# Kernel tuning notes

Measured on AMD Instinct MI355X. Metric: run time of the kernel, lower is better.

Reference implementation:

```python
import jax, jax.numpy as jnp
import numpy as np

N, F_IN, F_OUT = 20000, 512, 512
E = 320000
S = 6           # max_subgraph_size
T = 0.5         # evolution_time
HSCALE = 0.05   # Hamiltonian scale
MAX_TERMS = 4   # truncated matrix-exp series terms
EPS = 1e-5      # BatchNorm eps


def _build_subgraphs(edge_index_np):
    # deterministic stand-in for SubgraphCache: 1-hop in-neighbors, center first,
    # truncated to S nodes (matches mapping=0 after subsampling in the original)
    loops = np.stack([np.arange(N), np.arange(N)])
    ei = np.concatenate([edge_index_np.astype(np.int64), loops], axis=1)
    codes = np.unique(ei[0] * N + ei[1])   # dedup directed edges incl. self loops
    src, dst = codes // N, codes % N
    order = np.argsort(dst, kind='stable')
    src_s, dst_s = src[order], dst[order]
    starts = np.searchsorted(dst_s, np.arange(N))
    ends = np.searchsorted(dst_s, np.arange(N) + 1)
    sub_nodes = np.zeros((N, S), dtype=np.int32)
    valid = np.zeros((N, S), dtype=bool)
    for i in range(N):
        nb = np.unique(src_s[starts[i]:ends[i]])
        nb = nb[nb != i][:S - 1]
        k = 1 + nb.shape[0]
        sub_nodes[i, 0] = i
        sub_nodes[i, 1:k] = nb
        valid[i, :k] = True
    # induced directed adjacency of each size-S subgraph (padded slots zeroed)
    pair = sub_nodes[:, :, None].astype(np.int64) * N + sub_nodes[:, None, :].astype(np.int64)
    hit = np.isin(pair, codes)
    pv = valid[:, :, None] & valid[:, None, :]
    sub_adj = (hit & pv).astype(np.int32)
    return jnp.asarray(sub_nodes), jnp.asarray(sub_adj)


def setup_inputs() -> dict:
    key = jax.random.key(0)
    ks = jax.random.split(key, 4)
    x = jax.random.normal(ks[0], (N, F_IN), dtype=jnp.float32)
    edge_index = jax.random.randint(ks[1], (2, E), 0, N, dtype=jnp.int32)
    sub_nodes, sub_adj = _build_subgraphs(np.asarray(edge_index))
    W_re = jax.random.normal(ks[2], (F_IN, F_OUT), dtype=jnp.float32) * 0.02
    W_im = jax.random.normal(ks[3], (F_IN, F_OUT), dtype=jnp.float32) * 0.02
    b_re = jnp.zeros((F_OUT,), jnp.float32)
    b_im = jnp.zeros((F_OUT,), jnp.float32)
    gamma_r = jnp.ones((F_OUT,), jnp.float32)
    beta_r = jnp.zeros((F_OUT,), jnp.float32)
    gamma_i = jnp.ones((F_OUT,), jnp.float32)
    beta_i = jnp.zeros((F_OUT,), jnp.float32)
    return {"x": x, "edge_index": edge_index, "sub_nodes": sub_nodes,
            "sub_adj": sub_adj, "W_re": W_re, "W_im": W_im, "b_re": b_re,
            "b_im": b_im, "gamma_r": gamma_r, "beta_r": beta_r,
            "gamma_i": gamma_i, "beta_i": beta_i}


def _bn(v, gamma, beta):
    # training-mode BatchNorm1d (biased variance), applied per real/imag part
    mu = v.mean(axis=0)
    var = jnp.var(v, axis=0)
    return (v - mu) * jax.lax.rsqrt(var + EPS) * gamma + beta


def reference(x, edge_index, sub_nodes, sub_adj, W_re, W_im, b_re, b_im,
              gamma_r, beta_r, gamma_i, beta_i):
    # ComplexLinear on real-valued input: y = x @ (W_re + i W_im) + b
    y = jax.lax.complex(x @ W_re + b_re, x @ W_im + b_im)    # [N, F_OUT] c64
    # per-node subgraph Laplacian Hamiltonian: L = diag(deg) - A, H = 0.05 * L
    A = sub_adj.astype(jnp.float32)                          # [N, S, S]
    deg = A.sum(-1)                                          # degree(row)
    L = deg[:, :, None] * jnp.eye(S, dtype=jnp.float32) - A
    scaled = (-1j * T * HSCALE) * L.astype(jnp.complex64)    # -i * H * t
    # center row (index 0) of truncated series exp(-iHt); lower block of the
    # 2dim unitary hits zero-padded z rows, so only U_sub row 0 matters
    v = jnp.zeros((N, S), jnp.complex64).at[:, 0].set(1.0)
    term, res = v, v
    for k in range(1, MAX_TERMS + 1):
        term = jnp.einsum('ns,nst->nt', term, scaled) / k
        res = res + term
    sub_x = y[sub_nodes]                                     # [N, S, F_OUT]
    evolved = jnp.einsum('ns,nsf->nf', res, sub_x)           # center of U @ z
    # complex ReLU -> naive complex BatchNorm -> residual (in==out, no proj)
    er, ei = jax.nn.relu(evolved.real), jax.nn.relu(evolved.imag)
    out_r = _bn(er, gamma_r, beta_r) + x
    out_i = _bn(ei, gamma_i, beta_i)
    # complex output represented as concat(real, imag)
    return jnp.concatenate([out_r, out_i], axis=-1)          # [N, 2*F_OUT]
```

## Files before the change

kernel.cpp:

```cpp
#include <hip/hip_runtime.h>

#define N_NODES 20000
#define FDIM 512
#define SSZ 6

typedef __attribute__((ext_vector_type(8))) short bf16x8;
typedef __attribute__((ext_vector_type(4))) float f32x4;
typedef __attribute__((ext_vector_type(8))) unsigned short u16x8;

static __device__ __forceinline__ unsigned short f2bf(float f) {
    unsigned int u = __float_as_uint(f);
    unsigned int r = (u + 0x7fffu + ((u >> 16) & 1u)) >> 16;
    return (unsigned short)r;
}
static __device__ __forceinline__ float bf2f(unsigned short u) {
    return __uint_as_float(((unsigned int)u) << 16);
}

__global__ __launch_bounds__(256) void conv_all(
    const float* __restrict__ x, const float* __restrict__ Wre,
    const float* __restrict__ Wim, unsigned short* __restrict__ xb,
    unsigned short* __restrict__ wt, float* __restrict__ sums)
{
    const int blk = blockIdx.x;
    const int tid = threadIdx.x;
    if (blk < 5000) {
        const size_t i = ((size_t)blk * 256 + tid) * 8;
        const float4 a = *(const float4*)(x + i);
        const float4 b = *(const float4*)(x + i + 4);
        u16x8 o;
        o[0] = f2bf(a.x); o[1] = f2bf(a.y); o[2] = f2bf(a.z); o[3] = f2bf(a.w);
        o[4] = f2bf(b.x); o[5] = f2bf(b.y); o[6] = f2bf(b.z); o[7] = f2bf(b.w);
        *(u16x8*)(xb + i) = o;
    } else if (blk < 5512) {
        __shared__ float tile[32][33];
        const int bidx = blk - 5000;
        const int z = bidx >> 8;
        const int rem = bidx & 255;
        const int k0 = (rem & 15) * 32;
        const int n0 = (rem >> 4) * 32;
        const float* W = z ? Wim : Wre;
        const int tx = tid & 31, ty = tid >> 5;
#pragma unroll
        for (int i = 0; i < 4; ++i)
            tile[ty + i * 8][tx] = W[(size_t)(k0 + ty + i * 8) * FDIM + n0 + tx];
        __syncthreads();
        unsigned short* wtb = wt + (size_t)z * FDIM * FDIM;
#pragma unroll
        for (int i = 0; i < 4; ++i)
            wtb[(size_t)(n0 + ty + i * 8) * FDIM + k0 + tx] = f2bf(tile[tx][ty + i * 8]);
    } else {
#pragma unroll
        for (int i = 0; i < 8; ++i) sums[i * 256 + tid] = 0.f;
    }
}

#define BM 64
#define BN 128
#define BK 64

__global__ __launch_bounds__(256) void gemm_mfma(
    const unsigned short* __restrict__ xb,
    const unsigned short* __restrict__ wt,
    const float* __restrict__ bre, const float* __restrict__ bim,
    unsigned short* __restrict__ y)
{
    __shared__ __align__(16) unsigned short lA[BM * BK];
    __shared__ __align__(16) unsigned short lB[BN * BK];

    const int tid  = threadIdx.x;
    const int wave = tid >> 6;
    const int lane = tid & 63;
    const int rowBase = blockIdx.y * BM;
    const int colBase = blockIdx.x * BN;

    const int wm = (wave >> 1) * 32;
    const int wn = (wave & 1) * 64;

    f32x4 acc[2][4];
#pragma unroll
    for (int i = 0; i < 2; ++i)
#pragma unroll
        for (int j = 0; j < 4; ++j) acc[i][j] = (f32x4){0.f, 0.f, 0.f, 0.f};

    const int srow   = lane >> 3;
    const int schunk = lane & 7;
    const int gchunk = schunk ^ srow;

    const int fm = lane & 15;
    const int kq = lane >> 4;

    for (int k0 = 0; k0 < FDIM; k0 += BK) {
#pragma unroll
        for (int i = 0; i < 2; ++i) {
            const int trow = wave * 16 + i * 8;
            int grow = rowBase + trow + srow;
            if (grow > N_NODES - 1) grow = N_NODES - 1;
            const unsigned short* gp = xb + (size_t)grow * FDIM + k0 + gchunk * 8;
            __builtin_amdgcn_global_load_lds(
                (const __attribute__((address_space(1))) void*)gp,
                (__attribute__((address_space(3))) void*)(lA + trow * BK), 16, 0, 0);
        }
#pragma unroll
        for (int i = 0; i < 4; ++i) {
            const int trow = wave * 32 + i * 8;
            const int grow = colBase + trow + srow;
            const unsigned short* gp = wt + (size_t)grow * FDIM + k0 + gchunk * 8;
            __builtin_amdgcn_global_load_lds(
                (const __attribute__((address_space(1))) void*)gp,
                (__attribute__((address_space(3))) void*)(lB + trow * BK), 16, 0, 0);
        }
        __syncthreads();

#pragma unroll
        for (int ks = 0; ks < 2; ++ks) {
            bf16x8 af[2], bfr[4];
            const int g = ks * 4 + kq;
#pragma unroll
            for (int mt = 0; mt < 2; ++mt) {
                const int row = wm + mt * 16 + fm;
                af[mt] = *(const bf16x8*)&lA[row * BK + ((g ^ (row & 7)) << 3)];
            }
#pragma unroll
            for (int nt = 0; nt < 4; ++nt) {
                const int row = wn + nt * 16 + fm;
                bfr[nt] = *(const bf16x8*)&lB[row * BK + ((g ^ (row & 7)) << 3)];
            }
#pragma unroll
            for (int mt = 0; mt < 2; ++mt)
#pragma unroll
                for (int nt = 0; nt < 4; ++nt)
                    acc[mt][nt] = __builtin_amdgcn_mfma_f32_16x16x32_bf16(
                        af[mt], bfr[nt], acc[mt][nt], 0, 0, 0);
        }
        __syncthreads();
    }

    const int rquad = lane >> 4;
#pragma unroll
    for (int nt = 0; nt < 4; ++nt) {
        const int col = colBase + wn + nt * 16 + fm;
        const float bias = (col < FDIM) ? bre[col] : bim[col - FDIM];
#pragma unroll
        for (int mt = 0; mt < 2; ++mt) {
            const int row0 = rowBase + wm + mt * 16 + rquad * 4;
#pragma unroll
            for (int r = 0; r < 4; ++r) {
                const int row = row0 + r;
                if (row < N_NODES)
                    y[(size_t)row * 1024 + col] = f2bf(acc[mt][nt][r] + bias);
            }
        }
    }
}

__global__ __launch_bounds__(256) void evolve_stats(
    const unsigned short* __restrict__ y,
    const int* __restrict__ sub_nodes,
    const int* __restrict__ sub_adj,
    unsigned short* __restrict__ eb,
    float* __restrict__ sums)
{
    __shared__ float lsum[2048];
    const int wave = threadIdx.x >> 6;
    const int lane = threadIdx.x & 63;
    const int f = lane << 3;

    float sR[8] = {0.f}, sR2[8] = {0.f}, sI[8] = {0.f}, sI2[8] = {0.f};

    for (int q = 0; q < 4; ++q) {
        const int n = blockIdx.x * 16 + wave * 4 + q;

        const int* sa = sub_adj + (size_t)n * (SSZ * SSZ);
        float A[SSZ][SSZ], deg[SSZ];
#pragma unroll
        for (int s = 0; s < SSZ; ++s) {
            float d = 0.f;
#pragma unroll
            for (int t = 0; t < SSZ; ++t) { float a = (float)sa[s * SSZ + t]; A[s][t] = a; d += a; }
            deg[s] = d;
        }
        float p1[SSZ], p2[SSZ], p3[SSZ], p4[SSZ];
#pragma unroll
        for (int t = 0; t < SSZ; ++t) p1[t] = ((t == 0) ? deg[0] : 0.f) - A[0][t];
#pragma unroll
        for (int t = 0; t < SSZ; ++t) {
            float acc = 0.f;
#pragma unroll
            for (int s = 0; s < SSZ; ++s) acc += p1[s] * (((s == t) ? deg[s] : 0.f) - A[s][t]);
            p2[t] = acc;
        }
#pragma unroll
        for (int t = 0; t < SSZ; ++t) {
            float acc = 0.f;
#pragma unroll
            for (int s = 0; s < SSZ; ++s) acc += p2[s] * (((s == t) ? deg[s] : 0.f) - A[s][t]);
            p3[t] = acc;
        }
#pragma unroll
        for (int t = 0; t < SSZ; ++t) {
            float acc = 0.f;
#pragma unroll
            for (int s = 0; s < SSZ; ++s) acc += p3[s] * (((s == t) ? deg[s] : 0.f) - A[s][t]);
            p4[t] = acc;
        }
        float rre[SSZ], rim[SSZ];
#pragma unroll
        for (int t = 0; t < SSZ; ++t) {
            rre[t] = ((t == 0) ? 1.f : 0.f) - 3.125e-4f * p2[t] + 1.6276041666666668e-8f * p4[t];
            rim[t] = -0.025f * p1[t] + 2.6041666666666666e-6f * p3[t];
        }

        float aR[8] = {0.f}, aI[8] = {0.f};
#pragma unroll
        for (int s = 0; s < SSZ; ++s) {
            const int nd = sub_nodes[n * SSZ + s];
            const float cr = rre[s], ci = rim[s];
            const unsigned short* base = y + (size_t)nd * 1024 + f;
            const u16x8 yr8 = *(const u16x8*)base;
            const u16x8 yi8 = *(const u16x8*)(base + FDIM);
#pragma unroll
            for (int j = 0; j < 8; ++j) {
                const float yr = bf2f(yr8[j]);
                const float yi = bf2f(yi8[j]);
                aR[j] = fmaf(cr, yr, fmaf(-ci, yi, aR[j]));
                aI[j] = fmaf(cr, yi, fmaf(ci, yr, aI[j]));
            }
        }
        u16x8 er8, ei8;
#pragma unroll
        for (int j = 0; j < 8; ++j) {
            const unsigned short re = f2bf(fmaxf(aR[j], 0.f));
            const unsigned short im = f2bf(fmaxf(aI[j], 0.f));
            er8[j] = re; ei8[j] = im;
            const float erv = bf2f(re), eiv = bf2f(im);
            sR[j] += erv;  sR2[j] = fmaf(erv, erv, sR2[j]);
            sI[j] += eiv;  sI2[j] = fmaf(eiv, eiv, sI2[j]);
        }
        *(u16x8*)(eb + (size_t)n * 1024 + f) = er8;
        *(u16x8*)(eb + (size_t)n * 1024 + FDIM + f) = ei8;
    }

    if (wave == 0) {
#pragma unroll
        for (int j = 0; j < 8; ++j) {
            lsum[f + j] = sR[j];  lsum[512 + f + j] = sR2[j];
            lsum[1024 + f + j] = sI[j];  lsum[1536 + f + j] = sI2[j];
        }
    }
    for (int w = 1; w < 4; ++w) {
        __syncthreads();
        if (wave == w) {
#pragma unroll
            for (int j = 0; j < 8; ++j) {
                lsum[f + j] += sR[j];  lsum[512 + f + j] += sR2[j];
                lsum[1024 + f + j] += sI[j];  lsum[1536 + f + j] += sI2[j];
            }
        }
    }
    __syncthreads();
#pragma unroll
    for (int i = 0; i < 8; ++i) {
        const int idx = i * 256 + threadIdx.x;
        atomicAdd(&sums[idx], lsum[idx]);
    }
}

__global__ __launch_bounds__(256) void finalize_kernel(
    const float* __restrict__ x, const unsigned short* __restrict__ eb,
    const float* __restrict__ sums,
    const float* __restrict__ gr, const float* __restrict__ br_,
    const float* __restrict__ gi, const float* __restrict__ bi_,
    float* __restrict__ out)
{
    const int gid = blockIdx.x * 256 + threadIdx.x;
    const int n = gid >> 6;
    const int f = (gid & 63) << 3;
    const float invN = 1.0f / (float)N_NODES;

    float scr[8], shr[8], sci[8], shi[8];
#pragma unroll
    for (int h = 0; h < 2; ++h) {
        const int fo = f + h * 4;
        const float4 s1 = *(const float4*)(sums + fo);
        const float4 s2 = *(const float4*)(sums + 512 + fo);
        const float4 s3 = *(const float4*)(sums + 1024 + fo);
        const float4 s4 = *(const float4*)(sums + 1536 + fo);
        const float4 g1 = *(const float4*)(gr + fo);
        const float4 b1 = *(const float4*)(br_ + fo);
        const float4 g2 = *(const float4*)(gi + fo);
        const float4 b2 = *(const float4*)(bi_ + fo);
        const float mu[4] = {s1.x * invN, s1.y * invN, s1.z * invN, s1.w * invN};
        const float q2[4] = {s2.x * invN, s2.y * invN, s2.z * invN, s2.w * invN};
        const float mi[4] = {s3.x * invN, s3.y * invN, s3.z * invN, s3.w * invN};
        const float qi[4] = {s4.x * invN, s4.y * invN, s4.z * invN, s4.w * invN};
        const float gg1[4] = {g1.x, g1.y, g1.z, g1.w};
        const float bb1[4] = {b1.x, b1.y, b1.z, b1.w};
        const float gg2[4] = {g2.x, g2.y, g2.z, g2.w};
        const float bb2[4] = {b2.x, b2.y, b2.z, b2.w};
#pragma unroll
        for (int j = 0; j < 4; ++j) {
            const float vr = fmaf(-mu[j], mu[j], q2[j]);
            const float sc1 = rsqrtf(vr + 1e-5f) * gg1[j];
            scr[h * 4 + j] = sc1;
            shr[h * 4 + j] = fmaf(-mu[j], sc1, bb1[j]);
            const float vi = fmaf(-mi[j], mi[j], qi[j]);
            const float sc2 = rsqrtf(vi + 1e-5f) * gg2[j];
            sci[h * 4 + j] = sc2;
            shi[h * 4 + j] = fmaf(-mi[j], sc2, bb2[j]);
        }
    }

    const u16x8 er8 = *(const u16x8*)(eb + (size_t)n * 1024 + f);
    const u16x8 ei8 = *(const u16x8*)(eb + (size_t)n * 1024 + FDIM + f);
    float orr[8], oii[8];
#pragma unroll
    for (int j = 0; j < 8; ++j) {
        const float xv = x[(size_t)n * FDIM + f + j];
        orr[j] = fmaf(bf2f(er8[j]), scr[j], shr[j]) + xv;
        oii[j] = fmaf(bf2f(ei8[j]), sci[j], shi[j]);
    }
#pragma unroll
    for (int j = 0; j < 8; j += 4) {
        *(float4*)(out + (size_t)n * 1024 + f + j) =
            make_float4(orr[j], orr[j + 1], orr[j + 2], orr[j + 3]);
        *(float4*)(out + (size_t)n * 1024 + FDIM + f + j) =
            make_float4(oii[j], oii[j + 1], oii[j + 2], oii[j + 3]);
    }
}

extern "C" void kernel_launch(void* const* d_in, const int* in_sizes, int n_in,
                              void* d_out, int out_size, void* d_ws, size_t ws_size,
                              hipStream_t stream)
{
    const float* x        = (const float*)d_in[0];
    const int* sub_nodes  = (const int*)d_in[2];
    const int* sub_adj    = (const int*)d_in[3];
    const float* Wre      = (const float*)d_in[4];
    const float* Wim      = (const float*)d_in[5];
    const float* bre      = (const float*)d_in[6];
    const float* bim      = (const float*)d_in[7];
    const float* gr       = (const float*)d_in[8];
    const float* br_      = (const float*)d_in[9];
    const float* gi       = (const float*)d_in[10];
    const float* bi_      = (const float*)d_in[11];
    float* out = (float*)d_out;

    unsigned short* y  = (unsigned short*)d_ws;
    unsigned short* eb = y + (size_t)N_NODES * 1024;
    unsigned short* xb = eb + (size_t)N_NODES * 1024;
    unsigned short* wt = xb + (size_t)N_NODES * FDIM;
    float* sums        = (float*)(wt + (size_t)1024 * FDIM);

    conv_all<<<5513, 256, 0, stream>>>(x, Wre, Wim, xb, wt, sums);

    dim3 gg(1024 / BN, (N_NODES + BM - 1) / BM);
    gemm_mfma<<<gg, 256, 0, stream>>>(xb, wt, bre, bim, y);

    evolve_stats<<<N_NODES / 16, 256, 0, stream>>>(y, sub_nodes, sub_adj, eb, sums);

    finalize_kernel<<<(N_NODES * 64) / 256, 256, 0, stream>>>(
        x, eb, sums, gr, br_, gi, bi_, out);
}
```

Baseline: 248.8 us.

## Precompute per-node evolution coefficients and spread BN stat atomics across copies

The truncated matrix-exponential coefficients were recomputed by every lane of a wave for each node. They are now computed once per node in extra blocks of the conversion kernel and stored in a small coefficient buffer that the evolve kernel reads. The BatchNorm sum atomics are split over 8 replicated sum buffers, and the LDS reduction layout is changed to be lane-contiguous. A new single-block kernel reduces the copies into scale and shift parameters, so the finalize kernel no longer recomputes them for every element. The cost is an extra kernel launch and extra workspace; the bf16 input buffer now aliases the eb buffer, which is safe only because eb is written after the GEMM finishes.

```diff
diff --git a/kernel.cpp b/kernel.cpp
--- a/kernel.cpp
+++ b/kernel.cpp
@@ -3,6 +3,7 @@
 #define N_NODES 20000
 #define FDIM 512
 #define SSZ 6
+#define NCOPY 8
 
 typedef __attribute__((ext_vector_type(8))) short bf16x8;
 typedef __attribute__((ext_vector_type(4))) float f32x4;
@@ -19,8 +20,9 @@
 
 __global__ __launch_bounds__(256) void conv_all(
     const float* __restrict__ x, const float* __restrict__ Wre,
-    const float* __restrict__ Wim, unsigned short* __restrict__ xb,
-    unsigned short* __restrict__ wt, float* __restrict__ sums)
+    const float* __restrict__ Wim, const int* __restrict__ sub_adj,
+    unsigned short* __restrict__ xb, unsigned short* __restrict__ wt,
+    float* __restrict__ coef, float* __restrict__ sums)
 {
     const int blk = blockIdx.x;
     const int tid = threadIdx.x;
@@ -49,9 +51,54 @@
 #pragma unroll
         for (int i = 0; i < 4; ++i)
             wtb[(size_t)(n0 + ty + i * 8) * FDIM + k0 + tx] = f2bf(tile[tx][ty + i * 8]);
+    } else if (blk < 5591) {
+        const int c = (blk - 5512) * 256 + tid;
+        if (c < N_NODES) {
+            const int* sa = sub_adj + (size_t)c * (SSZ * SSZ);
+            float A[SSZ][SSZ], deg[SSZ];
+#pragma unroll
+            for (int s = 0; s < SSZ; ++s) {
+                float d = 0.f;
+#pragma unroll
+                for (int t = 0; t < SSZ; ++t) { float a = (float)sa[s * SSZ + t]; A[s][t] = a; d += a; }
+                deg[s] = d;
+            }
+            float p1[SSZ], p2[SSZ], p3[SSZ], p4[SSZ];
+#pragma unroll
+            for (int t = 0; t < SSZ; ++t) p1[t] = ((t == 0) ? deg[0] : 0.f) - A[0][t];
+#pragma unroll
+            for (int t = 0; t < SSZ; ++t) {
+                float acc = 0.f;
+#pragma unroll
+                for (int s = 0; s < SSZ; ++s) acc += p1[s] * (((s == t) ? deg[s] : 0.f) - A[s][t]);
+                p2[t] = acc;
+            }
+#pragma unroll
+            for (int t = 0; t < SSZ; ++t) {
+                float acc = 0.f;
+#pragma unroll
+                for (int s = 0; s < SSZ; ++s) acc += p2[s] * (((s == t) ? deg[s] : 0.f) - A[s][t]);
+                p3[t] = acc;
+            }
+#pragma unroll
+            for (int t = 0; t < SSZ; ++t) {
+                float acc = 0.f;
+#pragma unroll
+                for (int s = 0; s < SSZ; ++s) acc += p3[s] * (((s == t) ? deg[s] : 0.f) - A[s][t]);
+                p4[t] = acc;
+            }
+#pragma unroll
+            for (int t = 0; t < SSZ; ++t) {
+                coef[(size_t)c * 12 + t] =
+                    ((t == 0) ? 1.f : 0.f) - 3.125e-4f * p2[t] + 1.6276041666666668e-8f * p4[t];
+                coef[(size_t)c * 12 + 6 + t] =
+                    -0.025f * p1[t] + 2.6041666666666666e-6f * p3[t];
+            }
+        }
     } else {
-#pragma unroll
-        for (int i = 0; i < 8; ++i) sums[i * 256 + tid] = 0.f;
+        const int base = (blk - 5591) * 2048;
+#pragma unroll
+        for (int i = 0; i < 8; ++i) sums[base + i * 256 + tid] = 0.f;
     }
 }
 
@@ -157,7 +204,7 @@
 __global__ __launch_bounds__(256) void evolve_stats(
     const unsigned short* __restrict__ y,
     const int* __restrict__ sub_nodes,
-    const int* __restrict__ sub_adj,
+    const float* __restrict__ coef,
     unsigned short* __restrict__ eb,
     float* __restrict__ sums)
 {
@@ -170,52 +217,14 @@
 
     for (int q = 0; q < 4; ++q) {
         const int n = blockIdx.x * 16 + wave * 4 + q;
-
-        const int* sa = sub_adj + (size_t)n * (SSZ * SSZ);
-        float A[SSZ][SSZ], deg[SSZ];
+        const float* cp = coef + (size_t)n * 12;
+        const int* np = sub_nodes + n * SSZ;
+
+        float aR[8] = {0.f}, aI[8] = {0.f};
 #pragma unroll
         for (int s = 0; s < SSZ; ++s) {
-            float d = 0.f;
-#pragma unroll
-            for (int t = 0; t < SSZ; ++t) { float a = (float)sa[s * SSZ + t]; A[s][t] = a; d += a; }
-            deg[s] = d;
-        }
-        float p1[SSZ], p2[SSZ], p3[SSZ], p4[SSZ];
-#pragma unroll
-        for (int t = 0; t < SSZ; ++t) p1[t] = ((t == 0) ? deg[0] : 0.f) - A[0][t];
-#pragma unroll
-        for (int t = 0; t < SSZ; ++t) {
-            float acc = 0.f;
-#pragma unroll
-            for (int s = 0; s < SSZ; ++s) acc += p1[s] * (((s == t) ? deg[s] : 0.f) - A[s][t]);
-            p2[t] = acc;
-        }
-#pragma unroll
-        for (int t = 0; t < SSZ; ++t) {
-            float acc = 0.f;
-#pragma unroll
-            for (int s = 0; s < SSZ; ++s) acc += p2[s] * (((s == t) ? deg[s] : 0.f) - A[s][t]);
-            p3[t] = acc;
-        }
-#pragma unroll
-        for (int t = 0; t < SSZ; ++t) {
-            float acc = 0.f;
-#pragma unroll
-            for (int s = 0; s < SSZ; ++s) acc += p3[s] * (((s == t) ? deg[s] : 0.f) - A[s][t]);
-            p4[t] = acc;
-        }
-        float rre[SSZ], rim[SSZ];
-#pragma unroll
-        for (int t = 0; t < SSZ; ++t) {
-            rre[t] = ((t == 0) ? 1.f : 0.f) - 3.125e-4f * p2[t] + 1.6276041666666668e-8f * p4[t];
-            rim[t] = -0.025f * p1[t] + 2.6041666666666666e-6f * p3[t];
-        }
-
-        float aR[8] = {0.f}, aI[8] = {0.f};
-#pragma unroll
-        for (int s = 0; s < SSZ; ++s) {
-            const int nd = sub_nodes[n * SSZ + s];
-            const float cr = rre[s], ci = rim[s];
+            const float cr = cp[s], ci = cp[6 + s];
+            const int nd = np[s];
             const unsigned short* base = y + (size_t)nd * 1024 + f;
             const u16x8 yr8 = *(const u16x8*)base;
             const u16x8 yi8 = *(const u16x8*)(base + FDIM);
@@ -244,8 +253,10 @@
     if (wave == 0) {
 #pragma unroll
         for (int j = 0; j < 8; ++j) {
-            lsum[f + j] = sR[j];  lsum[512 + f + j] = sR2[j];
-            lsum[1024 + f + j] = sI[j];  lsum[1536 + f + j] = sI2[j];
+            lsum[j * 64 + lane] = sR[j];
+            lsum[512 + j * 64 + lane] = sR2[j];
+            lsum[1024 + j * 64 + lane] = sI[j];
+            lsum[1536 + j * 64 + lane] = sI2[j];
         }
     }
     for (int w = 1; w < 4; ++w) {
@@ -253,72 +264,69 @@
         if (wave == w) {
 #pragma unroll
             for (int j = 0; j < 8; ++j) {
-                lsum[f + j] += sR[j];  lsum[512 + f + j] += sR2[j];
-                lsum[1024 + f + j] += sI[j];  lsum[1536 + f + j] += sI2[j];
+                lsum[j * 64 + lane] += sR[j];
+                lsum[512 + j * 64 + lane] += sR2[j];
+                lsum[1024 + j * 64 + lane] += sI[j];
+                lsum[1536 + j * 64 + lane] += sI2[j];
             }
         }
     }
     __syncthreads();
+
+    float* sdst = sums + (blockIdx.x & (NCOPY - 1)) * 2048;
 #pragma unroll
     for (int i = 0; i < 8; ++i) {
         const int idx = i * 256 + threadIdx.x;
-        atomicAdd(&sums[idx], lsum[idx]);
-    }
-}
-
-__global__ __launch_bounds__(256) void finalize_kernel(
-    const float* __restrict__ x, const unsigned short* __restrict__ eb,
+        const int g = idx >> 9;
+        const int s = idx & 511;
+        const int feat = ((s & 63) << 3) + (s >> 6);
+        atomicAdd(&sdst[g * 512 + feat], lsum[idx]);
+    }
+}
+
+__global__ __launch_bounds__(512) void bnparams_kernel(
     const float* __restrict__ sums,
     const float* __restrict__ gr, const float* __restrict__ br_,
     const float* __restrict__ gi, const float* __restrict__ bi_,
-    float* __restrict__ out)
+    float* __restrict__ prm)
+{
+    const int f = threadIdx.x;
+    float s1 = 0.f, s2 = 0.f, s3 = 0.f, s4 = 0.f;
+#pragma unroll
+    for (int c = 0; c < NCOPY; ++c) {
+        const float* sc = sums + c * 2048;
+        s1 += sc[f]; s2 += sc[512 + f]; s3 += sc[1024 + f]; s4 += sc[1536 + f];
+    }
+    const float invN = 1.0f / (float)N_NODES;
+    const float mur = s1 * invN;
+    const float varr = fmaf(-mur, mur, s2 * invN);
+    const float scr = rsqrtf(varr + 1e-5f) * gr[f];
+    prm[f] = scr;
+    prm[512 + f] = fmaf(-mur, scr, br_[f]);
+    const float mui = s3 * invN;
+    const float vari = fmaf(-mui, mui, s4 * invN);
+    const float sci = rsqrtf(vari + 1e-5f) * gi[f];
+    prm[1024 + f] = sci;
+    prm[1536 + f] = fmaf(-mui, sci, bi_[f]);
+}
+
+__global__ __launch_bounds__(256) void finalize_kernel(
+    const float* __restrict__ x, const unsigned short* __restrict__ eb,
+    const float* __restrict__ prm, float* __restrict__ out)
 {
     const int gid = blockIdx.x * 256 + threadIdx.x;
     const int n = gid >> 6;
     const int f = (gid & 63) << 3;
-    const float invN = 1.0f / (float)N_NODES;
-
-    float scr[8], shr[8], sci[8], shi[8];
-#pragma unroll
-    for (int h = 0; h < 2; ++h) {
-        const int fo = f + h * 4;
-        const float4 s1 = *(const float4*)(sums + fo);
-        const float4 s2 = *(const float4*)(sums + 512 + fo);
-        const float4 s3 = *(const float4*)(sums + 1024 + fo);
-        const float4 s4 = *(const float4*)(sums + 1536 + fo);
-        const float4 g1 = *(const float4*)(gr + fo);
-        const float4 b1 = *(const float4*)(br_ + fo);
-        const float4 g2 = *(const float4*)(gi + fo);
-        const float4 b2 = *(const float4*)(bi_ + fo);
-        const float mu[4] = {s1.x * invN, s1.y * invN, s1.z * invN, s1.w * invN};
-        const float q2[4] = {s2.x * invN, s2.y * invN, s2.z * invN, s2.w * invN};
-        const float mi[4] = {s3.x * invN, s3.y * invN, s3.z * invN, s3.w * invN};
-        const float qi[4] = {s4.x * invN, s4.y * invN, s4.z * invN, s4.w * invN};
-        const float gg1[4] = {g1.x, g1.y, g1.z, g1.w};
-        const float bb1[4] = {b1.x, b1.y, b1.z, b1.w};
-        const float gg2[4] = {g2.x, g2.y, g2.z, g2.w};
-        const float bb2[4] = {b2.x, b2.y, b2.z, b2.w};
-#pragma unroll
-        for (int j = 0; j < 4; ++j) {
-            const float vr = fmaf(-mu[j], mu[j], q2[j]);
-            const float sc1 = rsqrtf(vr + 1e-5f) * gg1[j];
-            scr[h * 4 + j] = sc1;
-            shr[h * 4 + j] = fmaf(-mu[j], sc1, bb1[j]);
-            const float vi = fmaf(-mi[j], mi[j], qi[j]);
-            const float sc2 = rsqrtf(vi + 1e-5f) * gg2[j];
-            sci[h * 4 + j] = sc2;
-            shi[h * 4 + j] = fmaf(-mi[j], sc2, bb2[j]);
-        }
-    }
-
     const u16x8 er8 = *(const u16x8*)(eb + (size_t)n * 1024 + f);
     const u16x8 ei8 = *(const u16x8*)(eb + (size_t)n * 1024 + FDIM + f);
     float orr[8], oii[8];
 #pragma unroll
     for (int j = 0; j < 8; ++j) {
+        const float scr = prm[f + j],        shr = prm[512 + f + j];
+        const float sci = prm[1024 + f + j], shi = prm[1536 + f + j];
         const float xv = x[(size_t)n * FDIM + f + j];
-        orr[j] = fmaf(bf2f(er8[j]), scr[j], shr[j]) + xv;
-        oii[j] = fmaf(bf2f(ei8[j]), sci[j], shi[j]);
+        orr[j] = fmaf(bf2f(er8[j]), scr, shr) + xv;
+        oii[j] = fmaf(bf2f(ei8[j]), sci, shi);
     }
 #pragma unroll
     for (int j = 0; j < 8; j += 4) {
@@ -348,17 +356,20 @@
 
     unsigned short* y  = (unsigned short*)d_ws;
     unsigned short* eb = y + (size_t)N_NODES * 1024;
-    unsigned short* xb = eb + (size_t)N_NODES * 1024;
+    unsigned short* xb = eb;
     unsigned short* wt = xb + (size_t)N_NODES * FDIM;
-    float* sums        = (float*)(wt + (size_t)1024 * FDIM);
-
-    conv_all<<<5513, 256, 0, stream>>>(x, Wre, Wim, xb, wt, sums);
+    float* coef = (float*)(eb + (size_t)N_NODES * 1024);
+    float* sums = coef + (size_t)N_NODES * 12;
+    float* prm  = sums + NCOPY * 2048;
+
+    conv_all<<<5599, 256, 0, stream>>>(x, Wre, Wim, sub_adj, xb, wt, coef, sums);
 
     dim3 gg(1024 / BN, (N_NODES + BM - 1) / BM);
     gemm_mfma<<<gg, 256, 0, stream>>>(xb, wt, bre, bim, y);
 
-    evolve_stats<<<N_NODES / 16, 256, 0, stream>>>(y, sub_nodes, sub_adj, eb, sums);
-
-    finalize_kernel<<<(N_NODES * 64) / 256, 256, 0, stream>>>(
-        x, eb, sums, gr, br_, gi, bi_, out);
-}
+    evolve_stats<<<N_NODES / 16, 256, 0, stream>>>(y, sub_nodes, coef, eb, sums);
+
+    bnparams_kernel<<<1, 512, 0, stream>>>(sums, gr, br_, gi, bi_, prm);
+
+    finalize_kernel<<<(N_NODES * 64) / 256, 256, 0, stream>>>(x, eb, prm, out);
+}
```

Result: slower. 335.0 us (+34.7%).
